# Kernel optimization log

Hardware: AMD Instinct MI355X
Metric: run time of the kernel (lower is better)

The kernel has to match this reference:

```python
import jax, jax.numpy as jnp
import numpy as np

N_EMBD = 768
N_HEAD = 12
HEAD_DIM = N_EMBD // N_HEAD
EPS = 1e-5


def _ln(x, g, b):
    mu = jnp.mean(x, axis=-1, keepdims=True)
    var = jnp.mean(jnp.square(x - mu), axis=-1, keepdims=True)
    return (x - mu) * jax.lax.rsqrt(var + EPS) * g + b


def _gelu(x):
    # GPT-2 / BERT tanh-approximate GELU (new_gelu)
    c = jnp.sqrt(2.0 / jnp.pi).astype(x.dtype)
    return 0.5 * x * (1.0 + jnp.tanh(c * (x + 0.044715 * x * x * x)))


def setup_inputs() -> dict:
    key = jax.random.key(0)
    ks = jax.random.split(key, 8)
    B, T, C = 4, 2048, N_EMBD
    s = 0.02
    return {
        "x": jax.random.normal(ks[0], (B, T, C), jnp.float32),
        "attention_mask": jnp.ones((B, T), jnp.float32),
        "ln1_g": jnp.ones((C,), jnp.float32),
        "ln1_b": jnp.zeros((C,), jnp.float32),
        "ln2_g": jnp.ones((C,), jnp.float32),
        "ln2_b": jnp.zeros((C,), jnp.float32),
        "W_attn": jax.random.normal(ks[1], (C, 3 * C), jnp.float32) * s,
        "b_attn": jnp.zeros((3 * C,), jnp.float32),
        "W_proj": jax.random.normal(ks[2], (C, C), jnp.float32) * s,
        "b_proj": jnp.zeros((C,), jnp.float32),
        "W_fc": jax.random.normal(ks[3], (C, 4 * C), jnp.float32) * s,
        "b_fc": jnp.zeros((4 * C,), jnp.float32),
        "W_out": jax.random.normal(ks[4], (4 * C, C), jnp.float32) * s,
        "b_out": jnp.zeros((C,), jnp.float32),
    }


def reference(x, attention_mask, ln1_g, ln1_b, ln2_g, ln2_b,
              W_attn, b_attn, W_proj, b_proj, W_fc, b_fc, W_out, b_out):
    B, T, C = x.shape
    H, D = N_HEAD, HEAD_DIM

    # --- attention sublayer ---
    h = _ln(x, ln1_g, ln1_b)
    qkv = h @ W_attn + b_attn                      # [B,T,3C]
    q, k, v = jnp.split(qkv, 3, axis=-1)
    q = q.reshape(B, T, H, D).transpose(0, 2, 1, 3)  # [B,H,T,D]
    k = k.reshape(B, T, H, D).transpose(0, 2, 1, 3)
    v = v.reshape(B, T, H, D).transpose(0, 2, 1, 3)

    att = jnp.einsum('bhqd,bhkd->bhqk', q, k) * (1.0 / jnp.sqrt(D).astype(x.dtype))
    mask_add = (1.0 - attention_mask)[:, None, None, :] * -10000.0  # [B,1,1,T]
    att = att + mask_add
    att = jax.nn.softmax(att, axis=-1)
    y = jnp.einsum('bhqk,bhkd->bhqd', att, v)      # [B,H,T,D]
    y = y.transpose(0, 2, 1, 3).reshape(B, T, C)
    x = x + (y @ W_proj + b_proj)

    # --- MLP sublayer ---
    h = _ln(x, ln2_g, ln2_b)
    h = _gelu(h @ W_fc + b_fc)
    x = x + (h @ W_out + b_out)
    return x
```

## Files before the change

### kernel.cpp

```cpp
#include <hip/hip_runtime.h>
#include <hip/hip_bf16.h>
#include <cstdint>

using short8   = __attribute__((ext_vector_type(8))) short;
using floatx4  = __attribute__((ext_vector_type(4))) float;
using ushort4v = __attribute__((ext_vector_type(4))) unsigned short;

#define DEVI static __device__ __forceinline__

DEVI unsigned short f2bf(float f) {
    union { float f; unsigned u; } v; v.f = f;
    unsigned r = v.u + 0x7FFFu + ((v.u >> 16) & 1u);
    return (unsigned short)(r >> 16);
}

DEVI unsigned cvtpk_bf16(float lo, float hi) {
    unsigned r;
    asm("v_cvt_pk_bf16_f32 %0, %1, %2" : "=v"(r) : "v"(lo), "v"(hi));
    return r;
}

typedef const __attribute__((address_space(1))) unsigned int gas_uint;
typedef __attribute__((address_space(3))) unsigned int las_uint;

DEVI void gload16(const void* g, void* l) {
    __builtin_amdgcn_global_load_lds((gas_uint*)g, (las_uint*)l, 16, 0, 0);
}

DEVI float gelu_f(float x) {
    float z = 0.7978845608028654f * (x + 0.044715f * x * x * x);
    float e = __expf(2.0f * z);
    float t = 1.0f - 2.0f / (e + 1.0f);
    return 0.5f * x * (1.0f + t);
}

__global__ __launch_bounds__(256)
void transpose_cast(const float* __restrict__ W, unsigned short* __restrict__ Wt,
                    int K, int N)
{
    __shared__ float tile[32][33];
    const int n0 = blockIdx.x * 32, k0 = blockIdx.y * 32;
    const int tx = threadIdx.x & 31, ty = threadIdx.x >> 5;
#pragma unroll
    for (int j = 0; j < 4; ++j)
        tile[ty + j * 8][tx] = W[(long)(k0 + ty + j * 8) * N + n0 + tx];
    __syncthreads();
#pragma unroll
    for (int j = 0; j < 4; ++j)
        Wt[(long)(n0 + ty + j * 8) * K + k0 + tx] = f2bf(tile[tx][ty + j * 8]);
}

__global__ __launch_bounds__(256)
void ln_cast_k(const float* __restrict__ x, const float* __restrict__ g,
               const float* __restrict__ beta, unsigned short* __restrict__ out)
{
    const int row = blockIdx.x;
    const int tid = threadIdx.x;
    const float* xr = x + (long)row * 768;
    float v0 = xr[tid], v1 = xr[tid + 256], v2 = xr[tid + 512];
    float s  = v0 + v1 + v2;
    float sq = v0 * v0 + v1 * v1 + v2 * v2;
#pragma unroll
    for (int m = 1; m < 64; m <<= 1) {
        s  += __shfl_xor(s, m);
        sq += __shfl_xor(sq, m);
    }
    __shared__ float ss[4], ssq[4];
    if ((tid & 63) == 0) { ss[tid >> 6] = s; ssq[tid >> 6] = sq; }
    __syncthreads();
    s  = ss[0] + ss[1] + ss[2] + ss[3];
    sq = ssq[0] + ssq[1] + ssq[2] + ssq[3];
    const float mean = s * (1.0f / 768.0f);
    const float var  = sq * (1.0f / 768.0f) - mean * mean;
    const float rstd = rsqrtf(var + 1e-5f);
    unsigned short* orow = out + (long)row * 768;
    orow[tid]       = f2bf((v0 - mean) * rstd * g[tid]       + beta[tid]);
    orow[tid + 256] = f2bf((v1 - mean) * rstd * g[tid + 256] + beta[tid + 256]);
    orow[tid + 512] = f2bf((v2 - mean) * rstd * g[tid + 512] + beta[tid + 512]);
}

template<int EPI>
__global__ __launch_bounds__(256)
void gemm128(const unsigned short* __restrict__ A,
             const unsigned short* __restrict__ Bt,
             const float* __restrict__ bias,
             const float* __restrict__ resid,
             unsigned short* __restrict__ ob0,
             unsigned short* __restrict__ ob1,
             unsigned short* __restrict__ ob2,
             float* __restrict__ of,
             int K, int N)
{
    const int mt = blockIdx.x, nt = blockIdx.y;
    const int tid = threadIdx.x;
    const int w = tid >> 6, lane = tid & 63;
    const int l16 = lane & 15, lq = lane >> 4;
    const int wm = w >> 1, wn = w & 1;

    __shared__ unsigned short As[128 * 64];
    __shared__ unsigned short Bs[128 * 64];

    const floatx4 fzero = {0.f, 0.f, 0.f, 0.f};
    floatx4 acc[4][4];
#pragma unroll
    for (int i = 0; i < 4; ++i)
#pragma unroll
        for (int j = 0; j < 4; ++j) acc[i][j] = fzero;

    const char* Abyte = (const char*)A + (long)mt * 128 * K * 2;
    const char* Bbyte = (const char*)Bt + (long)nt * 128 * K * 2;
    const int KT = K >> 6;

    for (int kt = 0; kt < KT; ++kt) {
        const int kbyte = kt * 128;
#pragma unroll
        for (int r4 = 0; r4 < 4; ++r4) {
            int base = (w * 4 + r4) * 1024;
            int loff = base + lane * 16;
            int row  = loff >> 7;
            int scb  = (loff & 127) ^ ((row & 7) << 4);
            gload16(Abyte + (long)row * (K * 2) + kbyte + scb, (char*)As + base);
            gload16(Bbyte + (long)row * (K * 2) + kbyte + scb, (char*)Bs + base);
        }
        __syncthreads();
#pragma unroll
        for (int ks = 0; ks < 2; ++ks) {
            const int kb = ks * 64 + lq * 16;
            short8 af[4], bfr[4];
#pragma unroll
            for (int f = 0; f < 4; ++f) {
                int ar = wm * 64 + f * 16 + l16;
                af[f]  = *(const short8*)((const char*)As + ar * 128 + (kb ^ ((ar & 7) << 4)));
                int br = wn * 64 + f * 16 + l16;
                bfr[f] = *(const short8*)((const char*)Bs + br * 128 + (kb ^ ((br & 7) << 4)));
            }
#pragma unroll
            for (int i = 0; i < 4; ++i)
#pragma unroll
                for (int j = 0; j < 4; ++j)
                    acc[i][j] = __builtin_amdgcn_mfma_f32_16x16x32_bf16(af[i], bfr[j], acc[i][j], 0, 0, 0);
        }
        __syncthreads();
    }

    const int col0 = nt * 128 + wn * 64;
    const int row0 = mt * 128 + wm * 64;
#pragma unroll
    for (int j = 0; j < 4; ++j) {
        const int col = col0 + j * 16 + l16;
        const float bv = bias[col];
#pragma unroll
        for (int i = 0; i < 4; ++i) {
            const int rowb = row0 + i * 16 + lq * 4;
            float v[4];
#pragma unroll
            for (int r = 0; r < 4; ++r) v[r] = acc[i][j][r] + bv;

            if (EPI == 0) {
                const int which = (col >= 1536) ? 2 : (col >= 768 ? 1 : 0);
                const int c = col - which * 768;
                const int hh = c >> 6, d = c & 63;
                const int bb = rowb >> 11;
                const int t  = rowb & 2047;
                if (which == 2) {
                    ushort4v pk;
#pragma unroll
                    for (int r = 0; r < 4; ++r) pk[r] = f2bf(v[r]);
                    const int tlo = t & 31;
                    const int tS  = (t & ~31) + ((tlo & 12) << 1) + ((tlo & 16) >> 2);
                    long vi = ((long)(bb * 12 + hh) * 64 + d) * 2048 + tS;
                    *(ushort4v*)(ob2 + vi) = pk;
                } else {
                    unsigned short* dst = (which == 0) ? ob0 : ob1;
                    long base = ((long)(bb * 12 + hh) * 2048 + t) * 64 + d;
#pragma unroll
                    for (int r = 0; r < 4; ++r) dst[base + (long)r * 64] = f2bf(v[r]);
                }
            } else if (EPI == 1 || EPI == 3) {
#pragma unroll
                for (int r = 0; r < 4; ++r) {
                    long idx = (long)(rowb + r) * N + col;
                    of[idx] = v[r] + resid[idx];
                }
            } else {
#pragma unroll
                for (int r = 0; r < 4; ++r) {
                    long idx = (long)(rowb + r) * N + col;
                    ob0[idx] = f2bf(gelu_f(v[r]));
                }
            }
        }
    }
}

__global__ __launch_bounds__(256)
void attn_fwd(const unsigned short* __restrict__ q,
              const unsigned short* __restrict__ k,
              const unsigned short* __restrict__ vt,
              const float* __restrict__ mask,
              unsigned short* __restrict__ y)
{
    const int qt = blockIdx.x;
    const int bh = blockIdx.y;
    const int b = bh / 12, h = bh - b * 12;
    const int tid = threadIdx.x;
    const int w = tid >> 6, lane = tid & 63;
    const int l16 = lane & 15, lq = lane >> 4;

    __shared__ unsigned short Ks[128 * 64];
    __shared__ unsigned short Vs[64 * 128];
    __shared__ float madd[128];

    const char* kg = (const char*)(k + (long)bh * 2048 * 64);
    const char* vg = (const char*)(vt + (long)bh * 64 * 2048);

    const unsigned short* qrow = q + ((long)bh * 2048 + qt * 64 + w * 16 + l16) * 64;
    const short8 qf0 = *(const short8*)(qrow + lq * 8);
    const short8 qf1 = *(const short8*)(qrow + 32 + lq * 8);

    const floatx4 fzero = {0.f, 0.f, 0.f, 0.f};
    floatx4 accO[4];
#pragma unroll
    for (int n = 0; n < 4; ++n) accO[n] = fzero;
    float m2 = -1e30f, lsum = 0.f;
    const float sc2 = 0.125f * 1.4426950408889634f;

    for (int kt = 0; kt < 16; ++kt) {
#pragma unroll
        for (int r4 = 0; r4 < 4; ++r4) {
            int base = (w * 4 + r4) * 1024;
            int loff = base + lane * 16;
            int rowK = loff >> 7;
            int scbK = (loff & 127) ^ ((rowK & 7) << 4);
            gload16(kg + (long)(kt * 128 + rowK) * 128 + scbK, (char*)Ks + base);
            int rowV = loff >> 8;
            int scbV = (loff & 255) ^ ((rowV & 7) << 4);
            gload16(vg + (long)rowV * 4096 + kt * 256 + scbV, (char*)Vs + base);
        }
        if (tid < 128)
            madd[tid] = (1.0f - mask[b * 2048 + kt * 128 + tid]) * (-10000.0f * 1.4426950408889634f);
        __syncthreads();

        floatx4 st[8];
#pragma unroll
        for (int f = 0; f < 8; ++f) st[f] = fzero;
#pragma unroll
        for (int f = 0; f < 8; ++f) {
            const int kr = f * 16 + l16;
            const int sw = (kr & 7) << 4;
            short8 ka0 = *(const short8*)((const char*)Ks + kr * 128 + ((lq * 16) ^ sw));
            short8 ka1 = *(const short8*)((const char*)Ks + kr * 128 + ((64 + lq * 16) ^ sw));
            st[f] = __builtin_amdgcn_mfma_f32_16x16x32_bf16(ka0, qf0, st[f], 0, 0, 0);
            st[f] = __builtin_amdgcn_mfma_f32_16x16x32_bf16(ka1, qf1, st[f], 0, 0, 0);
        }

        float rm = -1e30f;
#pragma unroll
        for (int f = 0; f < 8; ++f) {
            floatx4 md = *(const floatx4*)((const char*)madd + f * 64 + lq * 16);
            floatx4 t;
#pragma unroll
            for (int j = 0; j < 4; ++j) {
                t[j] = st[f][j] * sc2 + md[j];
                rm = fmaxf(rm, t[j]);
            }
            st[f] = t;
        }
        rm = fmaxf(rm, __shfl_xor(rm, 16));
        rm = fmaxf(rm, __shfl_xor(rm, 32));
        const float mn = fmaxf(m2, rm);
        const float corr = exp2f(m2 - mn);
        m2 = mn;
        float rs = 0.f;
#pragma unroll
        for (int f = 0; f < 8; ++f) {
            floatx4 t = st[f];
#pragma unroll
            for (int j = 0; j < 4; ++j) {
                float p = exp2f(t[j] - mn);
                rs += p;
                t[j] = p;
            }
            st[f] = t;
        }
        rs += __shfl_xor(rs, 16);
        rs += __shfl_xor(rs, 32);
        lsum = lsum * corr + rs;

        const float c0 = __shfl(corr, lq * 4 + 0);
        const float c1 = __shfl(corr, lq * 4 + 1);
        const float c2 = __shfl(corr, lq * 4 + 2);
        const float c3 = __shfl(corr, lq * 4 + 3);
#pragma unroll
        for (int n = 0; n < 4; ++n) {
            floatx4 t = accO[n];
            t[0] *= c0; t[1] *= c1; t[2] *= c2; t[3] *= c3;
            accO[n] = t;
        }

#pragma unroll
        for (int c = 0; c < 4; ++c) {
            union { unsigned u[4]; short8 s8; } pu;
            pu.u[0] = cvtpk_bf16(st[2 * c][0],     st[2 * c][1]);
            pu.u[1] = cvtpk_bf16(st[2 * c][2],     st[2 * c][3]);
            pu.u[2] = cvtpk_bf16(st[2 * c + 1][0], st[2 * c + 1][1]);
            pu.u[3] = cvtpk_bf16(st[2 * c + 1][2], st[2 * c + 1][3]);
            const int kb2 = c * 64 + lq * 16;
#pragma unroll
            for (int n = 0; n < 4; ++n) {
                const int vr = n * 16 + l16;
                short8 vb = *(const short8*)((const char*)Vs + vr * 256 + (kb2 ^ ((vr & 7) << 4)));
                accO[n] = __builtin_amdgcn_mfma_f32_16x16x32_bf16(pu.s8, vb, accO[n], 0, 0, 0);
            }
        }
        __syncthreads();
    }

    const float li = 1.0f / lsum;
    const float li0 = __shfl(li, lq * 4 + 0);
    const float li1 = __shfl(li, lq * 4 + 1);
    const float li2 = __shfl(li, lq * 4 + 2);
    const float li3 = __shfl(li, lq * 4 + 3);
    const float lir[4] = {li0, li1, li2, li3};
    unsigned short* ybase = y + ((long)(b * 2048 + qt * 64 + w * 16 + lq * 4)) * 768 + h * 64;
#pragma unroll
    for (int r = 0; r < 4; ++r) {
        unsigned short* yrow = ybase + (long)r * 768;
#pragma unroll
        for (int n = 0; n < 4; ++n)
            yrow[n * 16 + l16] = f2bf(accO[n][r] * lir[r]);
    }
}

extern "C" void kernel_launch(void* const* d_in, const int* in_sizes, int n_in,
                              void* d_out, int out_size, void* d_ws, size_t ws_size,
                              hipStream_t stream)
{
    const float* x     = (const float*)d_in[0];
    const float* amask = (const float*)d_in[1];
    const float* ln1g  = (const float*)d_in[2];
    const float* ln1b  = (const float*)d_in[3];
    const float* ln2g  = (const float*)d_in[4];
    const float* ln2b  = (const float*)d_in[5];
    const float* Wattn = (const float*)d_in[6];
    const float* battn = (const float*)d_in[7];
    const float* Wproj = (const float*)d_in[8];
    const float* bproj = (const float*)d_in[9];
    const float* Wfc   = (const float*)d_in[10];
    const float* bfc   = (const float*)d_in[11];
    const float* Wout  = (const float*)d_in[12];
    const float* bout  = (const float*)d_in[13];
    float* out = (float*)d_out;

    char* ws = (char*)d_ws;
    unsigned short* wt_attn = (unsigned short*)ws;  ws += (long)2304 * 768 * 2;
    unsigned short* wt_proj = (unsigned short*)ws;  ws += (long)768 * 768 * 2;
    unsigned short* wt_fc   = (unsigned short*)ws;  ws += (long)3072 * 768 * 2;
    unsigned short* wt_out  = (unsigned short*)ws;  ws += (long)768 * 3072 * 2;
    unsigned short* hbuf    = (unsigned short*)ws;  ws += (long)8192 * 768 * 2;
    unsigned short* qbuf    = (unsigned short*)ws;  ws += (long)48 * 2048 * 64 * 2;
    unsigned short* kbuf    = (unsigned short*)ws;  ws += (long)48 * 2048 * 64 * 2;
    unsigned short* vtbuf   = (unsigned short*)ws;  ws += (long)48 * 2048 * 64 * 2;
    unsigned short* ybuf    = (unsigned short*)ws;  ws += (long)8192 * 768 * 2;
    unsigned short* hfc     = (unsigned short*)ws;  ws += (long)8192 * 3072 * 2;

    transpose_cast<<<dim3(2304 / 32, 768 / 32), 256, 0, stream>>>(Wattn, wt_attn, 768, 2304);
    transpose_cast<<<dim3(768 / 32, 768 / 32), 256, 0, stream>>>(Wproj, wt_proj, 768, 768);
    transpose_cast<<<dim3(3072 / 32, 768 / 32), 256, 0, stream>>>(Wfc, wt_fc, 768, 3072);
    transpose_cast<<<dim3(768 / 32, 3072 / 32), 256, 0, stream>>>(Wout, wt_out, 3072, 768);

    ln_cast_k<<<8192, 256, 0, stream>>>(x, ln1g, ln1b, hbuf);

    gemm128<0><<<dim3(64, 18), 256, 0, stream>>>(hbuf, wt_attn, battn, nullptr,
                                                 qbuf, kbuf, vtbuf, nullptr, 768, 2304);

    attn_fwd<<<dim3(32, 48), 256, 0, stream>>>(qbuf, kbuf, vtbuf, amask, ybuf);

    gemm128<1><<<dim3(64, 6), 256, 0, stream>>>(ybuf, wt_proj, bproj, x,
                                                nullptr, nullptr, nullptr, out, 768, 768);

    ln_cast_k<<<8192, 256, 0, stream>>>(out, ln2g, ln2b, hbuf);

    gemm128<2><<<dim3(64, 24), 256, 0, stream>>>(hbuf, wt_fc, bfc, nullptr,
                                                 hfc, nullptr, nullptr, nullptr, 768, 3072);

    gemm128<3><<<dim3(64, 6), 256, 0, stream>>>(hfc, wt_out, bout, out,
                                                nullptr, nullptr, nullptr, out, 3072, 768);
}
```

Before: 345.4 us.

## Process two query tiles per attention block, fold scale into Q, skip trivial mask

```diff
diff --git a/kernel.cpp b/kernel.cpp
--- a/kernel.cpp
+++ b/kernel.cpp
@@ -33,6 +33,8 @@
     float t = 1.0f - 2.0f / (e + 1.0f);
     return 0.5f * x * (1.0f + t);
 }
+
+#define QSCALE 0.18033688011112042f
 
 __global__ __launch_bounds__(256)
 void transpose_cast(const float* __restrict__ W, unsigned short* __restrict__ Wt,
@@ -172,9 +174,10 @@
                     *(ushort4v*)(ob2 + vi) = pk;
                 } else {
                     unsigned short* dst = (which == 0) ? ob0 : ob1;
+                    const float qs = (which == 0) ? QSCALE : 1.0f;
                     long base = ((long)(bb * 12 + hh) * 2048 + t) * 64 + d;
 #pragma unroll
-                    for (int r = 0; r < 4; ++r) dst[base + (long)r * 64] = f2bf(v[r]);
+                    for (int r = 0; r < 4; ++r) dst[base + (long)r * 64] = f2bf(v[r] * qs);
                 }
             } else if (EPI == 1 || EPI == 3) {
 #pragma unroll
@@ -191,6 +194,100 @@
             }
         }
     }
+}
+
+DEVI void attn_set(const unsigned short* Ks, const unsigned short* Vs,
+                   const float* madd, bool usemask,
+                   short8 qf0, short8 qf1,
+                   floatx4 (&acc)[4], float& m2, float& ls,
+                   int l16, int lq)
+{
+    const floatx4 fzero = {0.f, 0.f, 0.f, 0.f};
+    floatx4 st[8];
+#pragma unroll
+    for (int f = 0; f < 8; ++f) st[f] = fzero;
+
+    __builtin_amdgcn_s_setprio(1);
+#pragma unroll
+    for (int f = 0; f < 8; ++f) {
+        const int kr = f * 16 + l16;
+        const int sw = (kr & 7) << 4;
+        short8 ka0 = *(const short8*)((const char*)Ks + kr * 128 + ((lq * 16) ^ sw));
+        short8 ka1 = *(const short8*)((const char*)Ks + kr * 128 + ((64 + lq * 16) ^ sw));
+        st[f] = __builtin_amdgcn_mfma_f32_16x16x32_bf16(ka0, qf0, st[f], 0, 0, 0);
+        st[f] = __builtin_amdgcn_mfma_f32_16x16x32_bf16(ka1, qf1, st[f], 0, 0, 0);
+    }
+    __builtin_amdgcn_s_setprio(0);
+
+    if (usemask) {
+#pragma unroll
+        for (int f = 0; f < 8; ++f) {
+            floatx4 md = *(const floatx4*)((const char*)madd + f * 64 + lq * 16);
+            floatx4 t = st[f];
+#pragma unroll
+            for (int j = 0; j < 4; ++j) t[j] += md[j];
+            st[f] = t;
+        }
+    }
+
+    float rm = -3e38f;
+#pragma unroll
+    for (int f = 0; f < 8; ++f) {
+        rm = fmaxf(rm, fmaxf(fmaxf(st[f][0], st[f][1]), fmaxf(st[f][2], st[f][3])));
+    }
+    rm = fmaxf(rm, __shfl_xor(rm, 16));
+    rm = fmaxf(rm, __shfl_xor(rm, 32));
+
+    if (!__all(rm <= m2 + 8.0f)) {
+        const float mn = fmaxf(m2, rm);
+        const float corr = exp2f(m2 - mn);
+        m2 = mn;
+        ls *= corr;
+        const float c0 = __shfl(corr, lq * 4 + 0);
+        const float c1 = __shfl(corr, lq * 4 + 1);
+        const float c2 = __shfl(corr, lq * 4 + 2);
+        const float c3 = __shfl(corr, lq * 4 + 3);
+#pragma unroll
+        for (int n = 0; n < 4; ++n) {
+            floatx4 t = acc[n];
+            t[0] *= c0; t[1] *= c1; t[2] *= c2; t[3] *= c3;
+            acc[n] = t;
+        }
+    }
+
+    float rs = 0.f;
+#pragma unroll
+    for (int f = 0; f < 8; ++f) {
+        floatx4 t = st[f];
+#pragma unroll
+        for (int j = 0; j < 4; ++j) {
+            float p = exp2f(t[j] - m2);
+            rs += p;
+            t[j] = p;
+        }
+        st[f] = t;
+    }
+    rs += __shfl_xor(rs, 16);
+    rs += __shfl_xor(rs, 32);
+    ls += rs;
+
+    __builtin_amdgcn_s_setprio(1);
+#pragma unroll
+    for (int c = 0; c < 4; ++c) {
+        union { unsigned u[4]; short8 s8; } pu;
+        pu.u[0] = cvtpk_bf16(st[2 * c][0],     st[2 * c][1]);
+        pu.u[1] = cvtpk_bf16(st[2 * c][2],     st[2 * c][3]);
+        pu.u[2] = cvtpk_bf16(st[2 * c + 1][0], st[2 * c + 1][1]);
+        pu.u[3] = cvtpk_bf16(st[2 * c + 1][2], st[2 * c + 1][3]);
+        const int kb2 = c * 64 + lq * 16;
+#pragma unroll
+        for (int n = 0; n < 4; ++n) {
+            const int vr = n * 16 + l16;
+            short8 vb = *(const short8*)((const char*)Vs + vr * 256 + (kb2 ^ ((vr & 7) << 4)));
+            acc[n] = __builtin_amdgcn_mfma_f32_16x16x32_bf16(pu.s8, vb, acc[n], 0, 0, 0);
+        }
+    }
+    __builtin_amdgcn_s_setprio(0);
 }
 
 __global__ __launch_bounds__(256)
@@ -210,20 +307,34 @@
     __shared__ unsigned short Ks[128 * 64];
     __shared__ unsigned short Vs[64 * 128];
     __shared__ float madd[128];
+    __shared__ int mq;
 
     const char* kg = (const char*)(k + (long)bh * 2048 * 64);
     const char* vg = (const char*)(vt + (long)bh * 64 * 2048);
 
-    const unsigned short* qrow = q + ((long)bh * 2048 + qt * 64 + w * 16 + l16) * 64;
-    const short8 qf0 = *(const short8*)(qrow + lq * 8);
-    const short8 qf1 = *(const short8*)(qrow + 32 + lq * 8);
+    const unsigned short* qbase = q + ((long)bh * 2048 + qt * 128 + w * 16 + l16) * 64;
+    const short8 qfA0 = *(const short8*)(qbase + lq * 8);
+    const short8 qfA1 = *(const short8*)(qbase + 32 + lq * 8);
+    const short8 qfB0 = *(const short8*)(qbase + 64 * 64 + lq * 8);
+    const short8 qfB1 = *(const short8*)(qbase + 64 * 64 + 32 + lq * 8);
+
+    if (tid == 0) mq = 0;
+    __syncthreads();
+    {
+        const float* mrow = mask + (long)b * 2048 + tid * 8;
+        int bad = 0;
+#pragma unroll
+        for (int j = 0; j < 8; ++j) bad |= (mrow[j] != 1.0f);
+        if (bad) atomicOr(&mq, 1);
+    }
+    __syncthreads();
+    const bool usemask = (mq != 0);
 
     const floatx4 fzero = {0.f, 0.f, 0.f, 0.f};
-    floatx4 accO[4];
-#pragma unroll
-    for (int n = 0; n < 4; ++n) accO[n] = fzero;
-    float m2 = -1e30f, lsum = 0.f;
-    const float sc2 = 0.125f * 1.4426950408889634f;
+    floatx4 accA[4], accB[4];
+#pragma unroll
+    for (int n = 0; n < 4; ++n) { accA[n] = fzero; accB[n] = fzero; }
+    float m2A = -1e30f, lsA = 0.f, m2B = -1e30f, lsB = 0.f;
 
     for (int kt = 0; kt < 16; ++kt) {
 #pragma unroll
@@ -237,98 +348,33 @@
             int scbV = (loff & 255) ^ ((rowV & 7) << 4);
             gload16(vg + (long)rowV * 4096 + kt * 256 + scbV, (char*)Vs + base);
         }
-        if (tid < 128)
+        if (usemask && tid < 128)
             madd[tid] = (1.0f - mask[b * 2048 + kt * 128 + tid]) * (-10000.0f * 1.4426950408889634f);
         __syncthreads();
 
-        floatx4 st[8];
-#pragma unroll
-        for (int f = 0; f < 8; ++f) st[f] = fzero;
-#pragma unroll
-        for (int f = 0; f < 8; ++f) {
-            const int kr = f * 16 + l16;
-            const int sw = (kr & 7) << 4;
-            short8 ka0 = *(const short8*)((const char*)Ks + kr * 128 + ((lq * 16) ^ sw));
-            short8 ka1 = *(const short8*)((const char*)Ks + kr * 128 + ((64 + lq * 16) ^ sw));
-            st[f] = __builtin_amdgcn_mfma_f32_16x16x32_bf16(ka0, qf0, st[f], 0, 0, 0);
-            st[f] = __builtin_amdgcn_mfma_f32_16x16x32_bf16(ka1, qf1, st[f], 0, 0, 0);
-        }
-
-        float rm = -1e30f;
-#pragma unroll
-        for (int f = 0; f < 8; ++f) {
-            floatx4 md = *(const floatx4*)((const char*)madd + f * 64 + lq * 16);
-            floatx4 t;
-#pragma unroll
-            for (int j = 0; j < 4; ++j) {
-                t[j] = st[f][j] * sc2 + md[j];
-                rm = fmaxf(rm, t[j]);
-            }
-            st[f] = t;
-        }
-        rm = fmaxf(rm, __shfl_xor(rm, 16));
-        rm = fmaxf(rm, __shfl_xor(rm, 32));
-        const float mn = fmaxf(m2, rm);
-        const float corr = exp2f(m2 - mn);
-        m2 = mn;
-        float rs = 0.f;
-#pragma unroll
-        for (int f = 0; f < 8; ++f) {
-            floatx4 t = st[f];
-#pragma unroll
-            for (int j = 0; j < 4; ++j) {
-                float p = exp2f(t[j] - mn);
-                rs += p;
-                t[j] = p;
-            }
-            st[f] = t;
-        }
-        rs += __shfl_xor(rs, 16);
-        rs += __shfl_xor(rs, 32);
-        lsum = lsum * corr + rs;
-
-        const float c0 = __shfl(corr, lq * 4 + 0);
-        const float c1 = __shfl(corr, lq * 4 + 1);
-        const float c2 = __shfl(corr, lq * 4 + 2);
-        const float c3 = __shfl(corr, lq * 4 + 3);
-#pragma unroll
-        for (int n = 0; n < 4; ++n) {
-            floatx4 t = accO[n];
-            t[0] *= c0; t[1] *= c1; t[2] *= c2; t[3] *= c3;
-            accO[n] = t;
-        }
-
-#pragma unroll
-        for (int c = 0; c < 4; ++c) {
-            union { unsigned u[4]; short8 s8; } pu;
-            pu.u[0] = cvtpk_bf16(st[2 * c][0],     st[2 * c][1]);
-            pu.u[1] = cvtpk_bf16(st[2 * c][2],     st[2 * c][3]);
-            pu.u[2] = cvtpk_bf16(st[2 * c + 1][0], st[2 * c + 1][1]);
-            pu.u[3] = cvtpk_bf16(st[2 * c + 1][2], st[2 * c + 1][3]);
-            const int kb2 = c * 64 + lq * 16;
-#pragma unroll
-            for (int n = 0; n < 4; ++n) {
-                const int vr = n * 16 + l16;
-                short8 vb = *(const short8*)((const char*)Vs + vr * 256 + (kb2 ^ ((vr & 7) << 4)));
-                accO[n] = __builtin_amdgcn_mfma_f32_16x16x32_bf16(pu.s8, vb, accO[n], 0, 0, 0);
-            }
-        }
+        attn_set(Ks, Vs, madd, usemask, qfA0, qfA1, accA, m2A, lsA, l16, lq);
+        attn_set(Ks, Vs, madd, usemask, qfB0, qfB1, accB, m2B, lsB, l16, lq);
+
         __syncthreads();
     }
 
-    const float li = 1.0f / lsum;
-    const float li0 = __shfl(li, lq * 4 + 0);
-    const float li1 = __shfl(li, lq * 4 + 1);
-    const float li2 = __shfl(li, lq * 4 + 2);
-    const float li3 = __shfl(li, lq * 4 + 3);
-    const float lir[4] = {li0, li1, li2, li3};
-    unsigned short* ybase = y + ((long)(b * 2048 + qt * 64 + w * 16 + lq * 4)) * 768 + h * 64;
-#pragma unroll
-    for (int r = 0; r < 4; ++r) {
-        unsigned short* yrow = ybase + (long)r * 768;
-#pragma unroll
-        for (int n = 0; n < 4; ++n)
-            yrow[n * 16 + l16] = f2bf(accO[n][r] * lir[r]);
+#pragma unroll
+    for (int s = 0; s < 2; ++s) {
+        const float li = 1.0f / (s == 0 ? lsA : lsB);
+        const float li0 = __shfl(li, lq * 4 + 0);
+        const float li1 = __shfl(li, lq * 4 + 1);
+        const float li2 = __shfl(li, lq * 4 + 2);
+        const float li3 = __shfl(li, lq * 4 + 3);
+        const float lir[4] = {li0, li1, li2, li3};
+        const floatx4* acc = (s == 0) ? accA : accB;
+        unsigned short* ybase = y + ((long)(b * 2048 + qt * 128 + s * 64 + w * 16 + lq * 4)) * 768 + h * 64;
+#pragma unroll
+        for (int r = 0; r < 4; ++r) {
+            unsigned short* yrow = ybase + (long)r * 768;
+#pragma unroll
+            for (int n = 0; n < 4; ++n)
+                yrow[n * 16 + l16] = f2bf(acc[n][r] * lir[r]);
+        }
     }
 }
 
@@ -374,7 +420,7 @@
     gemm128<0><<<dim3(64, 18), 256, 0, stream>>>(hbuf, wt_attn, battn, nullptr,
                                                  qbuf, kbuf, vtbuf, nullptr, 768, 2304);
 
-    attn_fwd<<<dim3(32, 48), 256, 0, stream>>>(qbuf, kbuf, vtbuf, amask, ybuf);
+    attn_fwd<<<dim3(16, 48), 256, 0, stream>>>(qbuf, kbuf, vtbuf, amask, ybuf);
 
     gemm128<1><<<dim3(64, 6), 256, 0, stream>>>(ybuf, wt_proj, bproj, x,
                                                 nullptr, nullptr, nullptr, out, 768, 768);
```

Result: no change. 349.3 us (+1.1%).

## Fold softmax scale into Q, skip mask when all-ones, lazy rescale in attention

Applied to the files above, without the earlier changes.

```diff
diff --git a/kernel.cpp b/kernel.cpp
--- a/kernel.cpp
+++ b/kernel.cpp
@@ -33,6 +33,8 @@
     float t = 1.0f - 2.0f / (e + 1.0f);
     return 0.5f * x * (1.0f + t);
 }
+
+#define QSCALE 0.18033688011112042f
 
 __global__ __launch_bounds__(256)
 void transpose_cast(const float* __restrict__ W, unsigned short* __restrict__ Wt,
@@ -172,9 +174,10 @@
                     *(ushort4v*)(ob2 + vi) = pk;
                 } else {
                     unsigned short* dst = (which == 0) ? ob0 : ob1;
+                    const float qs = (which == 0) ? QSCALE : 1.0f;
                     long base = ((long)(bb * 12 + hh) * 2048 + t) * 64 + d;
 #pragma unroll
-                    for (int r = 0; r < 4; ++r) dst[base + (long)r * 64] = f2bf(v[r]);
+                    for (int r = 0; r < 4; ++r) dst[base + (long)r * 64] = f2bf(v[r] * qs);
                 }
             } else if (EPI == 1 || EPI == 3) {
 #pragma unroll
@@ -210,40 +213,61 @@
     __shared__ unsigned short Ks[128 * 64];
     __shared__ unsigned short Vs[64 * 128];
     __shared__ float madd[128];
-
-    const char* kg = (const char*)(k + (long)bh * 2048 * 64);
-    const char* vg = (const char*)(vt + (long)bh * 64 * 2048);
+    __shared__ int mq;
+
+    if (tid == 0) mq = 0;
+    __syncthreads();
+    {
+        const float* mrow = mask + (long)b * 2048 + tid * 8;
+        int bad = 0;
+#pragma unroll
+        for (int j = 0; j < 8; ++j) bad |= (mrow[j] != 1.0f);
+        if (bad) atomicOr(&mq, 1);
+    }
 
     const unsigned short* qrow = q + ((long)bh * 2048 + qt * 64 + w * 16 + l16) * 64;
     const short8 qf0 = *(const short8*)(qrow + lq * 8);
     const short8 qf1 = *(const short8*)(qrow + 32 + lq * 8);
 
+    const char* kg = (const char*)(k + (long)bh * 2048 * 64);
+    const char* vg = (const char*)(vt + (long)bh * 64 * 2048);
+    int koff[4], voff[4], lbase[4];
+#pragma unroll
+    for (int r4 = 0; r4 < 4; ++r4) {
+        int base = (w * 4 + r4) * 1024;
+        int loff = base + lane * 16;
+        int rowK = loff >> 7;
+        koff[r4] = rowK * 128 + ((loff & 127) ^ ((rowK & 7) << 4));
+        int rowV = loff >> 8;
+        voff[r4] = rowV * 4096 + ((loff & 255) ^ ((rowV & 7) << 4));
+        lbase[r4] = base;
+    }
+
+    __syncthreads();
+    const bool usemask = (mq != 0);
+
     const floatx4 fzero = {0.f, 0.f, 0.f, 0.f};
     floatx4 accO[4];
 #pragma unroll
     for (int n = 0; n < 4; ++n) accO[n] = fzero;
     float m2 = -1e30f, lsum = 0.f;
-    const float sc2 = 0.125f * 1.4426950408889634f;
 
     for (int kt = 0; kt < 16; ++kt) {
+        const char* kgt = kg + (long)kt * 16384;
+        const char* vgt = vg + kt * 256;
 #pragma unroll
         for (int r4 = 0; r4 < 4; ++r4) {
-            int base = (w * 4 + r4) * 1024;
-            int loff = base + lane * 16;
-            int rowK = loff >> 7;
-            int scbK = (loff & 127) ^ ((rowK & 7) << 4);
-            gload16(kg + (long)(kt * 128 + rowK) * 128 + scbK, (char*)Ks + base);
-            int rowV = loff >> 8;
-            int scbV = (loff & 255) ^ ((rowV & 7) << 4);
-            gload16(vg + (long)rowV * 4096 + kt * 256 + scbV, (char*)Vs + base);
-        }
-        if (tid < 128)
+            gload16(kgt + koff[r4], (char*)Ks + lbase[r4]);
+            gload16(vgt + voff[r4], (char*)Vs + lbase[r4]);
+        }
+        if (usemask && tid < 128)
             madd[tid] = (1.0f - mask[b * 2048 + kt * 128 + tid]) * (-10000.0f * 1.4426950408889634f);
         __syncthreads();
 
         floatx4 st[8];
 #pragma unroll
         for (int f = 0; f < 8; ++f) st[f] = fzero;
+        __builtin_amdgcn_s_setprio(1);
 #pragma unroll
         for (int f = 0; f < 8; ++f) {
             const int kr = f * 16 + l16;
@@ -253,58 +277,68 @@
             st[f] = __builtin_amdgcn_mfma_f32_16x16x32_bf16(ka0, qf0, st[f], 0, 0, 0);
             st[f] = __builtin_amdgcn_mfma_f32_16x16x32_bf16(ka1, qf1, st[f], 0, 0, 0);
         }
-
-        float rm = -1e30f;
-#pragma unroll
-        for (int f = 0; f < 8; ++f) {
-            floatx4 md = *(const floatx4*)((const char*)madd + f * 64 + lq * 16);
-            floatx4 t;
-#pragma unroll
-            for (int j = 0; j < 4; ++j) {
-                t[j] = st[f][j] * sc2 + md[j];
-                rm = fmaxf(rm, t[j]);
+        __builtin_amdgcn_s_setprio(0);
+
+        if (usemask) {
+#pragma unroll
+            for (int f = 0; f < 8; ++f) {
+                floatx4 md = *(const floatx4*)((const char*)madd + f * 64 + lq * 16);
+                floatx4 t = st[f];
+#pragma unroll
+                for (int j = 0; j < 4; ++j) t[j] += md[j];
+                st[f] = t;
             }
-            st[f] = t;
-        }
+        }
+
+        float rm = -3e38f;
+#pragma unroll
+        for (int f = 0; f < 8; ++f)
+            rm = fmaxf(rm, fmaxf(fmaxf(st[f][0], st[f][1]), fmaxf(st[f][2], st[f][3])));
         rm = fmaxf(rm, __shfl_xor(rm, 16));
         rm = fmaxf(rm, __shfl_xor(rm, 32));
-        const float mn = fmaxf(m2, rm);
-        const float corr = exp2f(m2 - mn);
-        m2 = mn;
+
+        if (!__all(rm <= m2 + 8.0f)) {
+            const float mn = fmaxf(m2, rm);
+            const float corr = exp2f(m2 - mn);
+            m2 = mn;
+            lsum *= corr;
+            const float c0 = __shfl(corr, lq * 4 + 0);
+            const float c1 = __shfl(corr, lq * 4 + 1);
+            const float c2 = __shfl(corr, lq * 4 + 2);
+            const float c3 = __shfl(corr, lq * 4 + 3);
+#pragma unroll
+            for (int n = 0; n < 4; ++n) {
+                floatx4 t = accO[n];
+                t[0] *= c0; t[1] *= c1; t[2] *= c2; t[3] *= c3;
+                accO[n] = t;
+            }
+        }
+
         float rs = 0.f;
+        unsigned pw[16];
 #pragma unroll
         for (int f = 0; f < 8; ++f) {
-            floatx4 t = st[f];
-#pragma unroll
-            for (int j = 0; j < 4; ++j) {
-                float p = exp2f(t[j] - mn);
-                rs += p;
-                t[j] = p;
-            }
-            st[f] = t;
+            const floatx4 t = st[f];
+            const float e0 = exp2f(t[0] - m2);
+            const float e1 = exp2f(t[1] - m2);
+            const float e2 = exp2f(t[2] - m2);
+            const float e3 = exp2f(t[3] - m2);
+            rs += (e0 + e1) + (e2 + e3);
+            pw[f * 2]     = cvtpk_bf16(e0, e1);
+            pw[f * 2 + 1] = cvtpk_bf16(e2, e3);
         }
         rs += __shfl_xor(rs, 16);
         rs += __shfl_xor(rs, 32);
-        lsum = lsum * corr + rs;
-
-        const float c0 = __shfl(corr, lq * 4 + 0);
-        const float c1 = __shfl(corr, lq * 4 + 1);
-        const float c2 = __shfl(corr, lq * 4 + 2);
-        const float c3 = __shfl(corr, lq * 4 + 3);
-#pragma unroll
-        for (int n = 0; n < 4; ++n) {
-            floatx4 t = accO[n];
-            t[0] *= c0; t[1] *= c1; t[2] *= c2; t[3] *= c3;
-            accO[n] = t;
-        }
-
+        lsum += rs;
+
+        __builtin_amdgcn_s_setprio(1);
 #pragma unroll
         for (int c = 0; c < 4; ++c) {
             union { unsigned u[4]; short8 s8; } pu;
-            pu.u[0] = cvtpk_bf16(st[2 * c][0],     st[2 * c][1]);
-            pu.u[1] = cvtpk_bf16(st[2 * c][2],     st[2 * c][3]);
-            pu.u[2] = cvtpk_bf16(st[2 * c + 1][0], st[2 * c + 1][1]);
-            pu.u[3] = cvtpk_bf16(st[2 * c + 1][2], st[2 * c + 1][3]);
+            pu.u[0] = pw[c * 4 + 0];
+            pu.u[1] = pw[c * 4 + 1];
+            pu.u[2] = pw[c * 4 + 2];
+            pu.u[3] = pw[c * 4 + 3];
             const int kb2 = c * 64 + lq * 16;
 #pragma unroll
             for (int n = 0; n < 4; ++n) {
@@ -313,6 +347,7 @@
                 accO[n] = __builtin_amdgcn_mfma_f32_16x16x32_bf16(pu.s8, vb, accO[n], 0, 0, 0);
             }
         }
+        __builtin_amdgcn_s_setprio(0);
         __syncthreads();
     }
 
```

New measurement: 341.3 us. No clear change (-1.2%).
